# Kernel tuning notes

Measured on AMD Instinct MI355X. Metric: run time of the kernel, lower is better.

Reference implementation:

```python
import jax, jax.numpy as jnp
import numpy as np

N = 500000      # active voxels
C_IN = 16       # input voxel feature dim
# encoder channels per stage: 32, 64, 128


def setup_inputs() -> dict:
    key = jax.random.key(0)
    ks = jax.random.split(key, 16)

    def w(k, i, o):
        return jax.random.normal(k, (i, o), dtype=jnp.float32) * (1.0 / np.sqrt(i))

    d = {}
    d['feat'] = jax.random.normal(ks[0], (N, C_IN), dtype=jnp.float32)
    d['coords'] = jax.random.randint(ks[1], (N, 4), 0, 1024, dtype=jnp.int32)
    d['W_in'] = w(ks[2], C_IN, 32)
    d['W_enc1'] = w(ks[3], 32, 32)
    d['W_enc2'] = w(ks[4], 32, 64)
    d['W_enc3'] = w(ks[5], 64, 128)
    d['W_lat1'] = w(ks[6], 32, 32)
    d['W_lat2'] = w(ks[7], 64, 64)
    d['W_lat3'] = w(ks[8], 128, 128)
    d['W_merge1'] = w(ks[9], 64, 32)    # merge: 2*C_i -> C_i
    d['W_merge2'] = w(ks[10], 128, 64)
    d['W_merge3'] = w(ks[11], 256, 128)
    d['W_up1'] = w(ks[12], 32, 32)      # upsample: C_i -> C_{i-1}
    d['W_up2'] = w(ks[13], 64, 32)
    d['W_up3'] = w(ks[14], 128, 64)
    return d


def _forward(feat, W_in, W_enc1, W_enc2, W_enc3, W_lat1, W_lat2, W_lat3,
             W_merge1, W_merge2, W_merge3, W_up1, W_up2, W_up3):
    relu = jax.nn.relu
    # conv_input + encoder (1x1 submanifold sparse convs == per-voxel matmul)
    x = relu(feat @ W_in)
    e1 = relu(x @ W_enc1)
    e2 = relu(e1 @ W_enc2)
    e3 = relu(e2 @ W_enc3)
    enc = [e1, e2, e3]
    lats = [W_lat1, W_lat2, W_lat3]
    mrgs = [W_merge1, W_merge2, W_merge3]
    ups = [W_up1, W_up2, W_up3]
    x = e3
    for i in (2, 1, 0):  # decoder stages stage_num..1
        lat = relu(enc[i] @ lats[i])                    # lateral_layer
        # cat0(x_bottom) + cat1(lat): identity-placement 1x1 convs == concat
        cat = jnp.concatenate([x, lat], axis=-1)        # [N, 2*C_i]
        merge = relu(cat @ mrgs[i])                     # merge_layer 2C->C
        red = cat.reshape(cat.shape[0], -1, 2).sum(-1)  # reduce_channel: fixed pairwise-sum conv
        x = relu((merge + red) @ ups[i])                # residual add + upsample_layer
    return x  # ret['voxel_feats']


def reference(feat, coords, W_in, W_enc1, W_enc2, W_enc3, W_lat1, W_lat2, W_lat3,
              W_merge1, W_merge2, W_merge3, W_up1, W_up2, W_up3):
    # coords define sparse structure; for 1x1 subm convs the math only touches features
    return _forward(feat, W_in, W_enc1, W_enc2, W_enc3, W_lat1, W_lat2, W_lat3,
                    W_merge1, W_merge2, W_merge3, W_up1, W_up2, W_up3)
```

## Files before the change

### kernel.cpp

```cpp
#include <hip/hip_runtime.h>

typedef unsigned short u16;
typedef unsigned int u32;
typedef _Float16 h16;
typedef __attribute__((ext_vector_type(2))) _Float16 half2v;
typedef __attribute__((ext_vector_type(8))) _Float16 half8;
typedef __attribute__((ext_vector_type(8))) unsigned short ushort8;
typedef __attribute__((ext_vector_type(4))) float f32x4;
typedef __attribute__((ext_vector_type(16))) float f32x16;

#define NPAIRS 15625
#define STRIPH 12032

#define AE1 0
#define SE1 40
#define AE2 1280
#define SE2 72
#define ACT 3584
#define SCT 264
#define AMR 3712
#define SMR 264

#define MFMA32(A,B,C) __builtin_amdgcn_mfma_f32_32x32x16_f16(A,B,C,0,0,0)

#define LBAR() asm volatile("s_waitcnt lgkmcnt(0)\n\ts_barrier" ::: "memory")
#define LWAIT() asm volatile("s_waitcnt lgkmcnt(0)" ::: "memory")

#define F_L0   0
#define F_L1   1
#define F_L2   3
#define F_L3   7
#define F_L4   23
#define F_L5   55
#define F_L6   119
#define F_L7   135
#define F_L8   143
#define F_L9   159
#define F_L10  163
#define F_L11  165
#define F_L12  169
#define NFRAG  171

__device__ __forceinline__ u16 hb(h16 h) { union { h16 h; u16 u; } v; v.h = h; return v.u; }

__global__ __launch_bounds__(256) void pack_w(
    const float* w0, const float* w1, const float* w2, const float* w3, const float* w4,
    const float* w5, const float* w6, const float* w7, const float* w8, const float* w9,
    const float* w10, const float* w11, const float* w12, u16* __restrict__ packed)
{
  const float* ws[13] = {w0,w1,w2,w3,w4,w5,w6,w7,w8,w9,w10,w11,w12};
  const int Ka[13]  = {16,32,32,64,128,256,128,64,128,64,32,64,32};
  const int KS[13]  = {1,2,2,4,8,16,8,4,8,4,2,4,2};
  const int CO[13]  = {32,32,64,128,128,128,64,64,64,32,32,32,32};
  const int FO[13]  = {F_L0,F_L1,F_L2,F_L3,F_L4,F_L5,F_L6,F_L7,F_L8,F_L9,F_L10,F_L11,F_L12};
  int g = blockIdx.x * 256 + threadIdx.x;
  int f = g >> 6, lane = g & 63;
  if (f >= NFRAG) return;
  int layer = 0;
#pragma unroll
  for (int i = 1; i < 13; ++i) if (f >= FO[i]) layer = i;
  int fl = f - FO[layer];
  int ks = fl % KS[layer];
  int ct = fl / KS[layer];
  int cout = CO[layer];
  int col  = ct * 32 + (lane & 31);
  u16 thi[8], tlo[8];
#pragma unroll
  for (int j = 0; j < 8; ++j) {
    int k = ks * 16 + (lane >> 5) * 8 + j;
    float w = (k < Ka[layer]) ? ws[layer][k * cout + col] : 0.f;
    h16 h = (h16)w;
    h16 l = (h16)(w - (float)h);
    thi[j] = hb(h); tlo[j] = hb(l);
  }
  u16* dst = packed + ((size_t)f * 64 + lane) * 16;
  *(ushort8*)dst       = *(const ushort8*)thi;
  *(ushort8*)(dst + 8) = *(const ushort8*)tlo;
}


struct fragp { half8 h, l; };

#define LOADFP(DST, BIDX)                                                       \
  do { const h16* _fp = wp + (((size_t)(BIDX)) * 64 + lane) * 16;               \
       (DST).h = *(const half8*)_fp; (DST).l = *(const half8*)(_fp + 8); } while (0)

#define PFC(FOFF, CIDX, KS_)                                                    \
  do { const int _fb = (FOFF) + (CIDX) * (KS_);                                 \
       LOADFP(pf0, _fb);                                                        \
       if ((KS_) > 1) LOADFP(pf1, _fb + 1);                                     \
       if ((KS_) > 2) LOADFP(pf2, _fb + 2);                                     \
       if ((KS_) > 3) LOADFP(pf3, _fb + 3); } while (0)

#define KSTEP(BP, KSI)                                                          \
  do { const h16* _p = asrc + abase + (KSI) * 16;                               \
       half8 _ah = *(const half8*)_p;                                           \
       half8 _al = *(const half8*)(_p + alo);                                   \
       accB = MFMA32(_al, (BP).h, accB);                                        \
       accA = MFMA32(_ah, (BP).h, accA);                                        \
       accB = MFMA32(_ah, (BP).l, accB); } while (0)

__device__ __forceinline__ void splitw(h16* dst, int idx, int dlo, float v) {
  h16 h = (h16)v;
  dst[idx]       = h;
  dst[idx + dlo] = (h16)(v - (float)h);
}

__device__ __forceinline__ float red2p(const h16* catS, int cs, int r16, int cc) {
  half2v hp = *reinterpret_cast<const half2v*>(catS + r16 * cs + 2 * cc);
  half2v lp = *reinterpret_cast<const half2v*>(catS + (r16 + 16) * cs + 2 * cc);
  return (float)hp.x + (float)hp.y + (float)lp.x + (float)lp.y;
}

template<int KS_, int EPI, int BAR>
__device__ __forceinline__ void layer32(
    const h16* __restrict__ asrc, int as,
    const h16* __restrict__ wp, int foff, int ct, int lane,
    fragp pf0, fragp pf1, fragp pf2, fragp pf3,
    h16* dst, int ds, int colb, const h16* cat, int cs,
    float* __restrict__ gout, int row0)
{
  const int ra = lane & 31;
  const int abase = (ra >> 4) * STRIPH + (ra & 15) * as + ((lane >> 5) << 3);
  const int alo = 16 * as;
  const int fb = foff + ct * KS_;
  f32x16 accA = {0.f,0.f,0.f,0.f,0.f,0.f,0.f,0.f,0.f,0.f,0.f,0.f,0.f,0.f,0.f,0.f};
  f32x16 accB = {0.f,0.f,0.f,0.f,0.f,0.f,0.f,0.f,0.f,0.f,0.f,0.f,0.f,0.f,0.f,0.f};
  fragp cur0 = pf0, cur1 = pf1, cur2 = pf2, cur3 = pf3;
  constexpr int NCH = (KS_ + 3) / 4;
#pragma unroll
  for (int ch = 0; ch < NCH; ++ch) {
    fragp nx0, nx1, nx2, nx3;
    if (ch + 1 < NCH) {
      const int nb = fb + (ch + 1) * 4;
      LOADFP(nx0, nb + 0); LOADFP(nx1, nb + 1);
      LOADFP(nx2, nb + 2); LOADFP(nx3, nb + 3);
    }
    const int k0 = ch * 4;
    if (k0 + 0 < KS_) KSTEP(cur0, k0 + 0);
    if (k0 + 1 < KS_) KSTEP(cur1, k0 + 1);
    if (k0 + 2 < KS_) KSTEP(cur2, k0 + 2);
    if (k0 + 3 < KS_) KSTEP(cur3, k0 + 3);
    if (ch + 1 < NCH) { cur0 = nx0; cur1 = nx1; cur2 = nx2; cur3 = nx3; }
  }
  const int cc  = ct * 32 + (lane & 31);
  const int hl4 = (lane >> 5) << 2;
  float vr[16];
#pragma unroll
  for (int i = 0; i < 16; ++i) {
    const int rr = (i & 3) + ((i >> 2) << 3) + hl4;
    float v = accA[i] + accB[i];
    v = v > 0.f ? v : 0.f;
    if (EPI == 1)
      v += red2p(cat + (rr >> 4) * STRIPH, cs, rr & 15, cc);
    vr[i] = v;
  }
  if (BAR) LBAR();
  if (EPI <= 1) {
    const int dlo = 16 * ds;
#pragma unroll
    for (int i = 0; i < 16; ++i) {
      const int rr = (i & 3) + ((i >> 2) << 3) + hl4;
      splitw(dst + (rr >> 4) * STRIPH, (rr & 15) * ds + colb + cc, dlo, vr[i]);
    }
  } else {
#pragma unroll
    for (int i = 0; i < 16; ++i) {
      const int rr = (i & 3) + ((i >> 2) << 3) + hl4;
      gout[(size_t)(row0 + rr) * 32 + cc] = vr[i];
    }
  }
}

__global__ __launch_bounds__(256, 3) void backbone(
    const float* __restrict__ feat, const h16* __restrict__ wp, float* __restrict__ out)
{
  __shared__ h16 lds[2 * STRIPH];
  const int lane = threadIdx.x & 63;
  const int wv   = threadIdx.x >> 6;
  const int row0 = blockIdx.x * 32;

  h16* E1 = lds + AE1;
  h16* E2 = lds + AE2;
  h16* CT = lds + ACT;
  h16* MR = lds + AMR;

  fragp pf0{}, pf1{}, pf2{}, pf3{};

  if (wv == 0) {
    PFC(F_L0, 0, 1);
    const int ra = lane & 31;
    const float* sp = feat + (size_t)(row0 + ra) * 16 + ((lane >> 5) << 3);
    f32x4 ua = *(const f32x4*)sp, ub = *(const f32x4*)(sp + 4);
    h16 th[8], tl[8];
#pragma unroll
    for (int j = 0; j < 4; ++j) {
      h16 h;
      h = (h16)ua[j]; th[j]   = h; tl[j]   = (h16)(ua[j] - (float)h);
      h = (h16)ub[j]; th[4+j] = h; tl[4+j] = (h16)(ub[j] - (float)h);
    }
    half8 ah = *(const half8*)th, al = *(const half8*)tl;
    f32x16 a = {0.f,0.f,0.f,0.f,0.f,0.f,0.f,0.f,0.f,0.f,0.f,0.f,0.f,0.f,0.f,0.f};
    a = MFMA32(al, pf0.h, a); a = MFMA32(ah, pf0.l, a); a = MFMA32(ah, pf0.h, a);
    const int cl = lane & 31, hl4 = (lane >> 5) << 2;
    const int dlo = 16 * SCT;
#pragma unroll
    for (int i = 0; i < 16; ++i) {
      const int rr = (i & 3) + ((i >> 2) << 3) + hl4;
      splitw(CT + (rr >> 4) * STRIPH, (rr & 15) * SCT + cl, dlo, a[i] > 0.f ? a[i] : 0.f);
    }
    PFC(F_L1, 0, 2);
    LWAIT();
    layer32<2,0,0>(CT, SCT, wp, F_L1, 0, lane, pf0,pf1,pf2,pf3,
                   E1, SE1, 0, nullptr, 0, nullptr, 0);
    PFC(F_L2, 0, 2);
  } else if (wv == 1) {
    PFC(F_L2, 1, 2);
  }
  LBAR();

  if (wv < 2) {
    layer32<2,0,0>(E1, SE1, wp, F_L2, wv, lane, pf0,pf1,pf2,pf3,
                   E2, SE2, 0, nullptr, 0, nullptr, 0);
  }
  PFC(F_L3, wv, 4);
  LBAR();

  layer32<4,0,0>(E2, SE2, wp, F_L3, wv, lane, pf0,pf1,pf2,pf3,
                 CT, SCT, 0, nullptr, 0, nullptr, 0);
  PFC(F_L4, wv, 8);
  LBAR();

  layer32<8,0,0>(CT, SCT, wp, F_L4, wv, lane, pf0,pf1,pf2,pf3,
                 CT, SCT, 128, nullptr, 0, nullptr, 0);
  PFC(F_L5, wv, 16);
  LBAR();

  layer32<16,1,1>(CT, SCT, wp, F_L5, wv, lane, pf0,pf1,pf2,pf3,
                  MR, SMR, 0, CT, SCT, nullptr, 0);
  if (wv < 2) PFC(F_L6, wv, 8); else PFC(F_L7, wv - 2, 4);
  LBAR();

  if (wv < 2) {
    layer32<8,0,0>(MR, SMR, wp, F_L6, wv, lane, pf0,pf1,pf2,pf3,
                   CT, SCT, 0, nullptr, 0, nullptr, 0);
    PFC(F_L8, wv, 8);
  } else {
    layer32<4,0,0>(E2, SE2, wp, F_L7, wv - 2, lane, pf0,pf1,pf2,pf3,
                   CT, SCT, 64, nullptr, 0, nullptr, 0);
  }
  LBAR();

  if (wv < 2) {
    layer32<8,1,0>(CT, SCT, wp, F_L8, wv, lane, pf0,pf1,pf2,pf3,
                   MR, SMR, 0, CT, SCT, nullptr, 0);
  }
  if (wv == 0) PFC(F_L9, 0, 4);
  else if (wv == 1) PFC(F_L10, 0, 2);
  LBAR();

  if (wv == 0) {
    layer32<4,0,0>(MR, SMR, wp, F_L9, 0, lane, pf0,pf1,pf2,pf3,
                   CT, SCT, 0, nullptr, 0, nullptr, 0);
    PFC(F_L11, 0, 4);
  } else if (wv == 1) {
    layer32<2,0,0>(E1, SE1, wp, F_L10, 0, lane, pf0,pf1,pf2,pf3,
                   CT, SCT, 32, nullptr, 0, nullptr, 0);
  }
  LBAR();

  if (wv == 0) {
    layer32<4,1,0>(CT, SCT, wp, F_L11, 0, lane, pf0,pf1,pf2,pf3,
                   MR, SMR, 0, CT, SCT, nullptr, 0);
    PFC(F_L12, 0, 2);
    LWAIT();
    layer32<2,2,0>(MR, SMR, wp, F_L12, 0, lane, pf0,pf1,pf2,pf3,
                   nullptr, 0, 0, nullptr, 0, out, row0);
  }
}

extern "C" void kernel_launch(void* const* d_in, const int* in_sizes, int n_in,
                              void* d_out, int out_size, void* d_ws, size_t ws_size,
                              hipStream_t stream) {
  (void)in_sizes; (void)n_in; (void)out_size; (void)ws_size;
  u16* packed = (u16*)d_ws;

  hipLaunchKernelGGL(pack_w, dim3(43), dim3(256), 0, stream,
      (const float*)d_in[2],  (const float*)d_in[3],  (const float*)d_in[4],
      (const float*)d_in[5],  (const float*)d_in[8],  (const float*)d_in[11],
      (const float*)d_in[14], (const float*)d_in[7],  (const float*)d_in[10],
      (const float*)d_in[13], (const float*)d_in[6],  (const float*)d_in[9],
      (const float*)d_in[12], packed);

  hipLaunchKernelGGL(backbone, dim3(NPAIRS), dim3(256), 0, stream,
                     (const float*)d_in[0], (const h16*)packed, (float*)d_out);
}
```

Baseline: 441.1 us.

## Spill e2 activations to global workspace to shrink LDS and raise occupancy

The e2 encoder activations (split fp16 hi/lo) are written to a per-block global workspace in MFMA-fragment layout instead of LDS. This shrinks the LDS strip from 12032 to 9728 halves and raises launch bounds from 3 to 4 blocks per CU. The consumers read the fragments directly from global memory, and a full vmcnt barrier orders the writes and reads. In exchange it adds global write and read traffic of about 64 MB, plus extra latency on two layers. It falls back to the old path if the workspace is too small.

```diff
diff --git a/kernel.cpp b/kernel.cpp
--- a/kernel.cpp
+++ b/kernel.cpp
@@ -10,20 +10,16 @@
 typedef __attribute__((ext_vector_type(16))) float f32x16;
 
 #define NPAIRS 15625
-#define STRIPH 12032
-
-#define AE1 0
+
 #define SE1 40
-#define AE2 1280
 #define SE2 72
-#define ACT 3584
 #define SCT 264
-#define AMR 3712
 #define SMR 264
 
 #define MFMA32(A,B,C) __builtin_amdgcn_mfma_f32_32x32x16_f16(A,B,C,0,0,0)
 
 #define LBAR() asm volatile("s_waitcnt lgkmcnt(0)\n\ts_barrier" ::: "memory")
+#define FBAR() asm volatile("s_waitcnt vmcnt(0) lgkmcnt(0)\n\ts_barrier" ::: "memory")
 #define LWAIT() asm volatile("s_waitcnt lgkmcnt(0)" ::: "memory")
 
 #define F_L0   0
@@ -40,6 +36,8 @@
 #define F_L11  165
 #define F_L12  169
 #define NFRAG  171
+#define EWS_OFF 350208
+#define EWS_BLK 4096
 
 __device__ __forceinline__ u16 hb(h16 h) { union { h16 h; u16 u; } v; v.h = h; return v.u; }
 
@@ -114,14 +112,14 @@
 
 template<int KS_, int EPI, int BAR>
 __device__ __forceinline__ void layer32(
-    const h16* __restrict__ asrc, int as,
+    const h16* __restrict__ asrc, int as, int strip,
     const h16* __restrict__ wp, int foff, int ct, int lane,
     fragp pf0, fragp pf1, fragp pf2, fragp pf3,
     h16* dst, int ds, int colb, const h16* cat, int cs,
     float* __restrict__ gout, int row0)
 {
   const int ra = lane & 31;
-  const int abase = (ra >> 4) * STRIPH + (ra & 15) * as + ((lane >> 5) << 3);
+  const int abase = (ra >> 4) * strip + (ra & 15) * as + ((lane >> 5) << 3);
   const int alo = 16 * as;
   const int fb = foff + ct * KS_;
   f32x16 accA = {0.f,0.f,0.f,0.f,0.f,0.f,0.f,0.f,0.f,0.f,0.f,0.f,0.f,0.f,0.f,0.f};
@@ -152,38 +150,84 @@
     float v = accA[i] + accB[i];
     v = v > 0.f ? v : 0.f;
     if (EPI == 1)
-      v += red2p(cat + (rr >> 4) * STRIPH, cs, rr & 15, cc);
+      v += red2p(cat + (rr >> 4) * strip, cs, rr & 15, cc);
     vr[i] = v;
   }
   if (BAR) LBAR();
-  if (EPI <= 1) {
+  if constexpr (EPI <= 1) {
     const int dlo = 16 * ds;
 #pragma unroll
     for (int i = 0; i < 16; ++i) {
       const int rr = (i & 3) + ((i >> 2) << 3) + hl4;
-      splitw(dst + (rr >> 4) * STRIPH, (rr & 15) * ds + colb + cc, dlo, vr[i]);
-    }
-  } else {
+      splitw(dst + (rr >> 4) * strip, (rr & 15) * ds + colb + cc, dlo, vr[i]);
+    }
+  } else if constexpr (EPI == 2) {
 #pragma unroll
     for (int i = 0; i < 16; ++i) {
       const int rr = (i & 3) + ((i >> 2) << 3) + hl4;
       gout[(size_t)(row0 + rr) * 32 + cc] = vr[i];
     }
-  }
-}
-
-__global__ __launch_bounds__(256, 3) void backbone(
-    const float* __restrict__ feat, const h16* __restrict__ wp, float* __restrict__ out)
+  } else {
+#pragma unroll
+    for (int i = 0; i < 16; ++i) {
+      const int rr = (i & 3) + ((i >> 2) << 3) + hl4;
+      const int sa = ((cc >> 4) << 10) + rr * 16 + (cc & 15);
+      h16 h = (h16)vr[i];
+      dst[sa]       = h;
+      dst[sa + 512] = (h16)(vr[i] - (float)h);
+    }
+  }
+}
+
+template<int KS_>
+__device__ __forceinline__ void layer32g(
+    const h16* __restrict__ esp, const h16* __restrict__ wp, int foff, int ct, int lane,
+    fragp pf0, fragp pf1, fragp pf2, fragp pf3,
+    h16* dst, int ds, int colb, int strip)
 {
-  __shared__ h16 lds[2 * STRIPH];
+  static_assert(KS_ <= 4, "layer32g handles one B chunk");
+  const int ab = (lane & 31) * 16 + ((lane >> 5) << 3);
+  half8 ah[KS_], al[KS_];
+#pragma unroll
+  for (int ks = 0; ks < KS_; ++ks) {
+    ah[ks] = *(const half8*)(esp + ks * 1024 + ab);
+    al[ks] = *(const half8*)(esp + ks * 1024 + 512 + ab);
+  }
+  f32x16 accA = {0.f,0.f,0.f,0.f,0.f,0.f,0.f,0.f,0.f,0.f,0.f,0.f,0.f,0.f,0.f,0.f};
+  f32x16 accB = {0.f,0.f,0.f,0.f,0.f,0.f,0.f,0.f,0.f,0.f,0.f,0.f,0.f,0.f,0.f,0.f};
+  if (KS_ > 0) { accB = MFMA32(al[0], pf0.h, accB); accA = MFMA32(ah[0], pf0.h, accA); accB = MFMA32(ah[0], pf0.l, accB); }
+  if (KS_ > 1) { accB = MFMA32(al[1], pf1.h, accB); accA = MFMA32(ah[1], pf1.h, accA); accB = MFMA32(ah[1], pf1.l, accB); }
+  if (KS_ > 2) { accB = MFMA32(al[2], pf2.h, accB); accA = MFMA32(ah[2], pf2.h, accA); accB = MFMA32(ah[2], pf2.l, accB); }
+  if (KS_ > 3) { accB = MFMA32(al[3], pf3.h, accB); accA = MFMA32(ah[3], pf3.h, accA); accB = MFMA32(ah[3], pf3.l, accB); }
+  const int cc  = ct * 32 + (lane & 31);
+  const int hl4 = (lane >> 5) << 2;
+  const int dlo = 16 * ds;
+#pragma unroll
+  for (int i = 0; i < 16; ++i) {
+    const int rr = (i & 3) + ((i >> 2) << 3) + hl4;
+    float v = accA[i] + accB[i];
+    v = v > 0.f ? v : 0.f;
+    splitw(dst + (rr >> 4) * strip, (rr & 15) * ds + colb + cc, dlo, v);
+  }
+}
+
+template<int SPILL>
+__global__ __launch_bounds__(256, 4) void backbone(
+    const float* __restrict__ feat, const h16* __restrict__ wp,
+    h16* __restrict__ ews, float* __restrict__ out)
+{
+  constexpr int STRIP = SPILL ? 9728 : 12032;
+  constexpr int ACTo  = SPILL ? 1280 : 3584;
+  __shared__ h16 lds[2 * STRIP];
   const int lane = threadIdx.x & 63;
   const int wv   = threadIdx.x >> 6;
   const int row0 = blockIdx.x * 32;
 
-  h16* E1 = lds + AE1;
-  h16* E2 = lds + AE2;
-  h16* CT = lds + ACT;
-  h16* MR = lds + AMR;
+  h16* E1 = lds;
+  h16* E2 = SPILL ? nullptr : (lds + 1280);
+  h16* CT = lds + ACTo;
+  h16* MR = CT + 128;
+  h16* esp = SPILL ? (ews + (size_t)blockIdx.x * EWS_BLK) : nullptr;
 
   fragp pf0{}, pf1{}, pf2{}, pf3{};
 
@@ -207,11 +251,11 @@
 #pragma unroll
     for (int i = 0; i < 16; ++i) {
       const int rr = (i & 3) + ((i >> 2) << 3) + hl4;
-      splitw(CT + (rr >> 4) * STRIPH, (rr & 15) * SCT + cl, dlo, a[i] > 0.f ? a[i] : 0.f);
+      splitw(CT + (rr >> 4) * STRIP, (rr & 15) * SCT + cl, dlo, a[i] > 0.f ? a[i] : 0.f);
     }
     PFC(F_L1, 0, 2);
     LWAIT();
-    layer32<2,0,0>(CT, SCT, wp, F_L1, 0, lane, pf0,pf1,pf2,pf3,
+    layer32<2,0,0>(CT, SCT, STRIP, wp, F_L1, 0, lane, pf0,pf1,pf2,pf3,
                    E1, SE1, 0, nullptr, 0, nullptr, 0);
     PFC(F_L2, 0, 2);
   } else if (wv == 1) {
@@ -220,39 +264,52 @@
   LBAR();
 
   if (wv < 2) {
-    layer32<2,0,0>(E1, SE1, wp, F_L2, wv, lane, pf0,pf1,pf2,pf3,
-                   E2, SE2, 0, nullptr, 0, nullptr, 0);
+    if constexpr (SPILL) {
+      layer32<2,3,0>(E1, SE1, STRIP, wp, F_L2, wv, lane, pf0,pf1,pf2,pf3,
+                     esp, 0, 0, nullptr, 0, nullptr, 0);
+    } else {
+      layer32<2,0,0>(E1, SE1, STRIP, wp, F_L2, wv, lane, pf0,pf1,pf2,pf3,
+                     E2, SE2, 0, nullptr, 0, nullptr, 0);
+    }
   }
   PFC(F_L3, wv, 4);
-  LBAR();
-
-  layer32<4,0,0>(E2, SE2, wp, F_L3, wv, lane, pf0,pf1,pf2,pf3,
-                 CT, SCT, 0, nullptr, 0, nullptr, 0);
+  if constexpr (SPILL) FBAR(); else LBAR();
+
+  if constexpr (SPILL) {
+    layer32g<4>(esp, wp, F_L3, wv, lane, pf0,pf1,pf2,pf3, CT, SCT, 0, STRIP);
+  } else {
+    layer32<4,0,0>(E2, SE2, STRIP, wp, F_L3, wv, lane, pf0,pf1,pf2,pf3,
+                   CT, SCT, 0, nullptr, 0, nullptr, 0);
+  }
   PFC(F_L4, wv, 8);
   LBAR();
 
-  layer32<8,0,0>(CT, SCT, wp, F_L4, wv, lane, pf0,pf1,pf2,pf3,
+  layer32<8,0,0>(CT, SCT, STRIP, wp, F_L4, wv, lane, pf0,pf1,pf2,pf3,
                  CT, SCT, 128, nullptr, 0, nullptr, 0);
   PFC(F_L5, wv, 16);
   LBAR();
 
-  layer32<16,1,1>(CT, SCT, wp, F_L5, wv, lane, pf0,pf1,pf2,pf3,
+  layer32<16,1,1>(CT, SCT, STRIP, wp, F_L5, wv, lane, pf0,pf1,pf2,pf3,
                   MR, SMR, 0, CT, SCT, nullptr, 0);
   if (wv < 2) PFC(F_L6, wv, 8); else PFC(F_L7, wv - 2, 4);
   LBAR();
 
   if (wv < 2) {
-    layer32<8,0,0>(MR, SMR, wp, F_L6, wv, lane, pf0,pf1,pf2,pf3,
+    layer32<8,0,0>(MR, SMR, STRIP, wp, F_L6, wv, lane, pf0,pf1,pf2,pf3,
                    CT, SCT, 0, nullptr, 0, nullptr, 0);
     PFC(F_L8, wv, 8);
   } else {
-    layer32<4,0,0>(E2, SE2, wp, F_L7, wv - 2, lane, pf0,pf1,pf2,pf3,
-                   CT, SCT, 64, nullptr, 0, nullptr, 0);
+    if constexpr (SPILL) {
+      layer32g<4>(esp, wp, F_L7, wv - 2, lane, pf0,pf1,pf2,pf3, CT, SCT, 64, STRIP);
+    } else {
+      layer32<4,0,0>(E2, SE2, STRIP, wp, F_L7, wv - 2, lane, pf0,pf1,pf2,pf3,
+                     CT, SCT, 64, nullptr, 0, nullptr, 0);
+    }
   }
   LBAR();
 
   if (wv < 2) {
-    layer32<8,1,0>(CT, SCT, wp, F_L8, wv, lane, pf0,pf1,pf2,pf3,
+    layer32<8,1,0>(CT, SCT, STRIP, wp, F_L8, wv, lane, pf0,pf1,pf2,pf3,
                    MR, SMR, 0, CT, SCT, nullptr, 0);
   }
   if (wv == 0) PFC(F_L9, 0, 4);
@@ -260,21 +317,21 @@
   LBAR();
 
   if (wv == 0) {
-    layer32<4,0,0>(MR, SMR, wp, F_L9, 0, lane, pf0,pf1,pf2,pf3,
+    layer32<4,0,0>(MR, SMR, STRIP, wp, F_L9, 0, lane, pf0,pf1,pf2,pf3,
                    CT, SCT, 0, nullptr, 0, nullptr, 0);
     PFC(F_L11, 0, 4);
   } else if (wv == 1) {
-    layer32<2,0,0>(E1, SE1, wp, F_L10, 0, lane, pf0,pf1,pf2,pf3,
+    layer32<2,0,0>(E1, SE1, STRIP, wp, F_L10, 0, lane, pf0,pf1,pf2,pf3,
                    CT, SCT, 32, nullptr, 0, nullptr, 0);
   }
   LBAR();
 
   if (wv == 0) {
-    layer32<4,1,0>(CT, SCT, wp, F_L11, 0, lane, pf0,pf1,pf2,pf3,
+    layer32<4,1,0>(CT, SCT, STRIP, wp, F_L11, 0, lane, pf0,pf1,pf2,pf3,
                    MR, SMR, 0, CT, SCT, nullptr, 0);
     PFC(F_L12, 0, 2);
     LWAIT();
-    layer32<2,2,0>(MR, SMR, wp, F_L12, 0, lane, pf0,pf1,pf2,pf3,
+    layer32<2,2,0>(MR, SMR, STRIP, wp, F_L12, 0, lane, pf0,pf1,pf2,pf3,
                    nullptr, 0, 0, nullptr, 0, out, row0);
   }
 }
@@ -282,8 +339,10 @@
 extern "C" void kernel_launch(void* const* d_in, const int* in_sizes, int n_in,
                               void* d_out, int out_size, void* d_ws, size_t ws_size,
                               hipStream_t stream) {
-  (void)in_sizes; (void)n_in; (void)out_size; (void)ws_size;
+  (void)in_sizes; (void)n_in; (void)out_size;
   u16* packed = (u16*)d_ws;
+  h16* ews = (h16*)((char*)d_ws + EWS_OFF);
+  const bool spill = ws_size >= (size_t)EWS_OFF + (size_t)NPAIRS * EWS_BLK * 2;
 
   hipLaunchKernelGGL(pack_w, dim3(43), dim3(256), 0, stream,
       (const float*)d_in[2],  (const float*)d_in[3],  (const float*)d_in[4],
@@ -292,6 +351,11 @@
       (const float*)d_in[13], (const float*)d_in[6],  (const float*)d_in[9],
       (const float*)d_in[12], packed);
 
-  hipLaunchKernelGGL(backbone, dim3(NPAIRS), dim3(256), 0, stream,
-                     (const float*)d_in[0], (const h16*)packed, (float*)d_out);
-}
+  if (spill) {
+    hipLaunchKernelGGL((backbone<1>), dim3(NPAIRS), dim3(256), 0, stream,
+                       (const float*)d_in[0], (const h16*)packed, ews, (float*)d_out);
+  } else {
+    hipLaunchKernelGGL((backbone<0>), dim3(NPAIRS), dim3(256), 0, stream,
+                       (const float*)d_in[0], (const h16*)packed, (h16*)nullptr, (float*)d_out);
+  }
+}
```

After: 450.0 us. 1.02x slower.
